# Performance work log

Measured on AMD Instinct MI355X. Metric: run time of the kernel, lower is better.

## Reference

```python
import jax, jax.numpy as jnp
import numpy as np

EPS = 1e-8

def setup_inputs() -> dict:
    key = jax.random.key(0)
    k0, k1, k2, k3, k4 = jax.random.split(key, 5)
    B, N, K, Q, L, F = 8, 5, 5, 4, 128, 768
    support_emb = jax.random.normal(k0, (B, N, K, L, F), dtype=jnp.float32)
    query_emb = jax.random.normal(k1, (B, N * Q, L, F), dtype=jnp.float32)
    B_mask = jax.random.randint(k2, (B, N, K, L), 0, 2, dtype=jnp.int32)
    I_mask = jax.random.randint(k3, (B, N, K, L), 0, 2, dtype=jnp.int32)
    trigger_label = jax.random.randint(k4, (B, N * Q, L), 0, 2 * N + 1, dtype=jnp.int32)
    return {"support_emb": support_emb, "query_emb": query_emb, "B_mask": B_mask,
            "I_mask": I_mask, "trigger_label": trigger_label, "N": N, "K": K, "Q": Q}

def _proto(support_emb, Bm, Im, N):
    # support_emb: (B,N,K,L,F); Bm/Im: (B,N,K,L) float
    sum_B = jnp.einsum('bnklf,bnkl->bnf', support_emb, Bm)
    cnt_B = Bm.sum((2, 3))[..., None] + EPS
    pB = sum_B / cnt_B                                   # (B,N,F)
    sum_I = jnp.einsum('bnklf,bnkl->bnf', support_emb, Im)
    cnt_I = Im.sum((2, 3))[..., None] + EPS
    pI = sum_I / cnt_I                                   # (B,N,F)
    Om = 1.0 - Bm - Im                                   # (B,N,K,L)
    sum_O = jnp.einsum('bnklf,bnkl->bf', support_emb, Om)
    cnt_O = Om.sum((1, 2, 3))[:, None] + EPS
    pO = sum_O / cnt_O                                   # (B,F)
    Bsz, F = pO.shape
    # interleave: tags [O, B_0, I_0, B_1, I_1, ...]
    pBI = jnp.stack([pB, pI], axis=2).reshape(Bsz, 2 * N, F)
    return jnp.concatenate([pO[:, None, :], pBI], axis=1)  # (B, 2N+1, F)

def reference(support_emb, query_emb, B_mask, I_mask, trigger_label, N, K, Q):
    dt = support_emb.dtype
    Bm = B_mask.astype(dt)
    Im = I_mask.astype(dt)
    prototype = _proto(support_emb, Bm, Im, N)             # (B, 2N+1, F)
    # similarity: broadcast dot product -> batched GEMM
    logits = jnp.einsum('bqlf,btf->bqlt', query_emb, prototype)  # (B, NQ, L, 2N+1)
    T = logits.shape[-1]
    flat = logits.reshape(-1, T)
    pred = jnp.argmax(flat, axis=1)
    lab = trigger_label.reshape(-1)
    logp = jax.nn.log_softmax(flat, axis=-1)
    loss = -jnp.take_along_axis(logp, lab[:, None], axis=1).mean()
    return (loss, logits, pred)
```

## Files before the change

### kernel.cpp

```cpp
#include <hip/hip_runtime.h>
#include <cstdint>
#include <cstddef>

#define EPS 1e-8f

#define Bsz 8
#define Nn  5
#define Kk  5
#define Ll  128
#define Ff  768
#define Tt  11
#define KL  640
#define ROWS_PER_B 2560
#define NROWS 20480
#define F4  192
#define BN  40

#define S1_ROWS 64
#define S1_CH   (KL / S1_ROWS)
#define S1_NBLK (BN * S1_CH)
#define PART_STRIDE (3 * Ff)
#define PART_STRIDE4 (PART_STRIDE / 4)

typedef float v2f __attribute__((ext_vector_type(2)));

__global__ __launch_bounds__(192) void stage1(
    const float* __restrict__ sup,
    const int*   __restrict__ Bm,
    const int*   __restrict__ Im,
    float* __restrict__ part,
    float* __restrict__ pcnt)
{
    int blk = blockIdx.x;
    int bn  = blk / S1_CH;
    int ch  = blk - bn * S1_CH;
    int tid = threadIdx.x;

    const float4* sp = (const float4*)(sup + ((size_t)bn * KL + ch * S1_ROWS) * Ff) + tid;
    const int*    bp = Bm + bn * KL + ch * S1_ROWS;
    const int*    ip = Im + bn * KL + ch * S1_ROWS;

    v2f tB0 = {0.f,0.f}, tB1 = tB0, tI0 = tB0, tI1 = tB0, tA0 = tB0, tA1 = tB0;
    int cB = 0, cI = 0;

    for (int h = 0; h < S1_ROWS / 8; ++h) {
        float4 v[8];
        #pragma unroll
        for (int j = 0; j < 8; ++j) v[j] = sp[(size_t)(h * 8 + j) * F4];
        #pragma unroll
        for (int j = 0; j < 8; ++j) {
            int p = h * 8 + j;
            v2f lo = {v[j].x, v[j].y};
            v2f hi = {v[j].z, v[j].w};
            tA0 += lo; tA1 += hi;
            if (bp[p]) { tB0 += lo; tB1 += hi; ++cB; }
            if (ip[p]) { tI0 += lo; tI1 += hi; ++cI; }
        }
    }

    float4* o = (float4*)(part + (size_t)blk * PART_STRIDE);
    float4 rB = {tB0.x, tB0.y, tB1.x, tB1.y};
    float4 rI = {tI0.x, tI0.y, tI1.x, tI1.y};
    float4 rA = {tA0.x, tA0.y, tA1.x, tA1.y};
    o[tid]          = rB;
    o[F4 + tid]     = rI;
    o[2 * F4 + tid] = rA;

    if (tid == 0) {
        pcnt[2 * (size_t)blk]     = (float)cB;
        pcnt[2 * (size_t)blk + 1] = (float)cI;
    }
}

__global__ __launch_bounds__(256) void stage2(
    const float* __restrict__ part,
    const float* __restrict__ pcnt,
    float* __restrict__ bnsum,
    float* __restrict__ cnt,
    float* __restrict__ loss_out)
{
    int gid = blockIdx.x * 256 + threadIdx.x;
    if (gid == 0) loss_out[0] = 0.0f;

    int bn  = gid / (3 * F4);
    int r   = gid - bn * (3 * F4);
    int set = r / F4;
    int f4  = r - set * F4;

    const float4* src = (const float4*)part + ((size_t)bn * S1_CH * 3 + set) * F4 + f4;
    float4 s = {0, 0, 0, 0};
    float4 v[S1_CH];
    #pragma unroll
    for (int c = 0; c < S1_CH; ++c) v[c] = src[(size_t)c * PART_STRIDE4];
    #pragma unroll
    for (int c = 0; c < S1_CH; ++c) {
        s.x += v[c].x; s.y += v[c].y; s.z += v[c].z; s.w += v[c].w;
    }
    ((float4*)bnsum)[((size_t)bn * 3 + set) * F4 + f4] = s;

    if (gid < 2 * BN) {
        int bn2  = gid >> 1;
        int set2 = gid & 1;
        float cv = 0.0f;
        #pragma unroll
        for (int c = 0; c < S1_CH; ++c) cv += pcnt[2 * ((size_t)bn2 * S1_CH + c) + set2];
        cnt[gid] = cv;
    }
}

__global__ __launch_bounds__(192) void stage2b(
    const float* __restrict__ bnsum,
    const float* __restrict__ cnt,
    float* __restrict__ proto)
{
    int b  = blockIdx.x / Tt;
    int t  = blockIdx.x - b * Tt;
    int f4 = threadIdx.x;

    const float4* bs = (const float4*)bnsum + (size_t)b * Nn * 3 * F4;

    float scale;
    if (t == 0) {
        float cO = (float)(KL * Nn);
        #pragma unroll
        for (int k = 0; k < 2 * Nn; ++k) cO -= cnt[2 * Nn * b + k];
        scale = 1.0f / (cO + EPS);
    } else {
        scale = 1.0f / (cnt[2 * Nn * b + (t - 1)] + EPS);
    }

    float4 val;
    if (t == 0) {
        float sx = 0, sy = 0, sz = 0, sw = 0;
        #pragma unroll
        for (int n = 0; n < Nn; ++n) {
            float4 A  = bs[(n * 3 + 2) * F4 + f4];
            float4 Bv = bs[(n * 3 + 0) * F4 + f4];
            float4 Iv = bs[(n * 3 + 1) * F4 + f4];
            sx += A.x - Bv.x - Iv.x; sy += A.y - Bv.y - Iv.y;
            sz += A.z - Bv.z - Iv.z; sw += A.w - Bv.w - Iv.w;
        }
        val.x = sx; val.y = sy; val.z = sz; val.w = sw;
    } else {
        int n  = (t - 1) >> 1;
        int st = (t - 1) & 1;
        val = bs[(n * 3 + st) * F4 + f4];
    }
    val.x *= scale; val.y *= scale; val.z *= scale; val.w *= scale;
    ((float4*)proto)[((size_t)b * Tt + t) * F4 + f4] = val;
}

#define S3_ROWS 64
#define S3_NBLK (NROWS / S3_ROWS)

__global__ __launch_bounds__(256) void stage3(
    const float* __restrict__ query,
    const float* __restrict__ proto,
    const int*   __restrict__ label,
    float* __restrict__ out_logits,
    float* __restrict__ out_pred,
    float* __restrict__ loss_out)
{
    __shared__ float4 ldsP[Tt * F4];
    __shared__ float  lred[4];

    int blk = blockIdx.x;
    int tid = threadIdx.x;
    int b   = blk / (ROWS_PER_B / S3_ROWS);

    const float4* pp = (const float4*)proto + (size_t)b * Tt * F4;
    for (int idx = tid; idx < Tt * F4; idx += 256) ldsP[idx] = pp[idx];
    __syncthreads();

    int p = tid >> 4;
    int s = tid & 15;

    size_t row0 = (size_t)blk * S3_ROWS + p * 4;
    const float4* qb = (const float4*)query + row0 * F4 + s;

    float a0[Tt], a1[Tt], a2[Tt], a3[Tt];
    #pragma unroll
    for (int t = 0; t < Tt; ++t) { a0[t] = 0.f; a1[t] = 0.f; a2[t] = 0.f; a3[t] = 0.f; }

    float4 u0 = qb[0 * F4], u1 = qb[1 * F4], u2 = qb[2 * F4], u3 = qb[3 * F4];

    const float4* pb = ldsP + s;
    #pragma unroll
    for (int j = 0; j < 12; ++j) {
        float4 w0, w1, w2, w3;
        if (j < 11) {
            int o = (j + 1) * 16;
            w0 = qb[0 * F4 + o]; w1 = qb[1 * F4 + o];
            w2 = qb[2 * F4 + o]; w3 = qb[3 * F4 + o];
        }
        #pragma unroll
        for (int t = 0; t < Tt; ++t) {
            float4 pv = pb[t * F4 + j * 16];
            float d0 = a0[t], d1 = a1[t], d2 = a2[t], d3 = a3[t];
            d0 = fmaf(u0.x, pv.x, d0); d0 = fmaf(u0.y, pv.y, d0);
            d0 = fmaf(u0.z, pv.z, d0); d0 = fmaf(u0.w, pv.w, d0);
            d1 = fmaf(u1.x, pv.x, d1); d1 = fmaf(u1.y, pv.y, d1);
            d1 = fmaf(u1.z, pv.z, d1); d1 = fmaf(u1.w, pv.w, d1);
            d2 = fmaf(u2.x, pv.x, d2); d2 = fmaf(u2.y, pv.y, d2);
            d2 = fmaf(u2.z, pv.z, d2); d2 = fmaf(u2.w, pv.w, d2);
            d3 = fmaf(u3.x, pv.x, d3); d3 = fmaf(u3.y, pv.y, d3);
            d3 = fmaf(u3.z, pv.z, d3); d3 = fmaf(u3.w, pv.w, d3);
            a0[t] = d0; a1[t] = d1; a2[t] = d2; a3[t] = d3;
        }
        if (j < 11) { u0 = w0; u1 = w1; u2 = w2; u3 = w3; }
    }

    #pragma unroll
    for (int t = 0; t < Tt; ++t) {
        a0[t] += __shfl_xor(a0[t], 1, 16); a0[t] += __shfl_xor(a0[t], 2, 16);
        a0[t] += __shfl_xor(a0[t], 4, 16); a0[t] += __shfl_xor(a0[t], 8, 16);
        a1[t] += __shfl_xor(a1[t], 1, 16); a1[t] += __shfl_xor(a1[t], 2, 16);
        a1[t] += __shfl_xor(a1[t], 4, 16); a1[t] += __shfl_xor(a1[t], 8, 16);
        a2[t] += __shfl_xor(a2[t], 1, 16); a2[t] += __shfl_xor(a2[t], 2, 16);
        a2[t] += __shfl_xor(a2[t], 4, 16); a2[t] += __shfl_xor(a2[t], 8, 16);
        a3[t] += __shfl_xor(a3[t], 1, 16); a3[t] += __shfl_xor(a3[t], 2, 16);
        a3[t] += __shfl_xor(a3[t], 4, 16); a3[t] += __shfl_xor(a3[t], 8, 16);
    }

    float wloss = 0.0f;
    if (s < 4) {
        float rv[Tt];
        #pragma unroll
        for (int t = 0; t < Tt; ++t)
            rv[t] = (s == 0) ? a0[t] : (s == 1) ? a1[t] : (s == 2) ? a2[t] : a3[t];
        size_t grow = row0 + s;

        float m = rv[0]; int bt = 0;
        #pragma unroll
        for (int t = 1; t < Tt; ++t) if (rv[t] > m) { m = rv[t]; bt = t; }
        float sum = 0.0f;
        #pragma unroll
        for (int t = 0; t < Tt; ++t) sum += __expf(rv[t] - m);
        int lab = label[grow];
        float labv = rv[0];
        #pragma unroll
        for (int t = 1; t < Tt; ++t) labv = (lab == t) ? rv[t] : labv;
        #pragma unroll
        for (int t = 0; t < Tt; ++t) out_logits[grow * Tt + t] = rv[t];
        out_pred[grow] = (float)bt;
        wloss = (m + __logf(sum)) - labv;
    }
    #pragma unroll
    for (int off = 32; off > 0; off >>= 1) wloss += __shfl_xor(wloss, off, 64);
    if ((tid & 63) == 0) lred[tid >> 6] = wloss;
    __syncthreads();
    if (tid == 0)
        atomicAdd(loss_out, (lred[0] + lred[1] + lred[2] + lred[3]) * (1.0f / (float)NROWS));
}

extern "C" void kernel_launch(void* const* d_in, const int* in_sizes, int n_in,
                              void* d_out, int out_size, void* d_ws, size_t ws_size,
                              hipStream_t stream) {
    const float* sup   = (const float*)d_in[0];
    const float* query = (const float*)d_in[1];
    const int*   Bm    = (const int*)d_in[2];
    const int*   Im    = (const int*)d_in[3];
    const int*   lab   = (const int*)d_in[4];

    float* w     = (float*)d_ws;
    float* part  = w;
    float* pcnt  = part + (size_t)S1_NBLK * PART_STRIDE;
    float* bnsum = pcnt + 2 * S1_NBLK;
    float* cnt   = bnsum + (size_t)BN * 3 * Ff;
    float* proto = cnt + 2 * BN;

    float* loss_out   = (float*)d_out;
    float* out_logits = (float*)d_out + 1;
    float* out_pred   = (float*)d_out + 1 + (size_t)NROWS * Tt;

    stage1<<<S1_NBLK, 192, 0, stream>>>(sup, Bm, Im, part, pcnt);
    stage2<<<90, 256, 0, stream>>>(part, pcnt, bnsum, cnt, loss_out);
    stage2b<<<Bsz * Tt, 192, 0, stream>>>(bnsum, cnt, proto);
    stage3<<<S3_NBLK, 256, 0, stream>>>(query, proto, lab,
                                        out_logits, out_pred, loss_out);
}
```

Baseline: 195.5 us.

## Widen stage1 blocks, fuse stage2 kernels, and raise stage3 rows per thread

Stage1 now runs four 192-thread row groups per block and reduces their partials in shared memory, giving more loads in flight per block. The two small prototype kernels are merged into one kernel that keeps per-batch sums in LDS, which removes a launch and a global round trip. Stage3 now has each thread accumulate 8 rows instead of 4 in 128-thread blocks, so each prototype value read from LDS is reused across twice as many rows. The cost is much higher register pressure in stage3 (88 accumulators plus 16 float4 query buffers), which could lower occupancy or cause spills.

Result: no change. 195.5 us, median of 2 (+0.0%).

```diff
diff --git a/kernel.cpp b/kernel.cpp
--- a/kernel.cpp
+++ b/kernel.cpp
@@ -17,6 +17,8 @@
 #define BN  40
 
 #define S1_ROWS 64
+#define S1_G    4
+#define S1_GR   16
 #define S1_CH   (KL / S1_ROWS)
 #define S1_NBLK (BN * S1_CH)
 #define PART_STRIDE (3 * Ff)
@@ -24,26 +26,33 @@
 
 typedef float v2f __attribute__((ext_vector_type(2)));
 
-__global__ __launch_bounds__(192) void stage1(
+__global__ __launch_bounds__(768) void stage1(
     const float* __restrict__ sup,
     const int*   __restrict__ Bm,
     const int*   __restrict__ Im,
     float* __restrict__ part,
     float* __restrict__ pcnt)
 {
+    __shared__ float4 red[S1_G * 3 * F4];
+    __shared__ float  redc[S1_G * 2];
+
     int blk = blockIdx.x;
     int bn  = blk / S1_CH;
     int ch  = blk - bn * S1_CH;
     int tid = threadIdx.x;
-
-    const float4* sp = (const float4*)(sup + ((size_t)bn * KL + ch * S1_ROWS) * Ff) + tid;
-    const int*    bp = Bm + bn * KL + ch * S1_ROWS;
-    const int*    ip = Im + bn * KL + ch * S1_ROWS;
+    int g   = tid / 192;
+    int col = tid - g * 192;
+    int rbase = ch * S1_ROWS + g * S1_GR;
+
+    const float4* sp = (const float4*)(sup + ((size_t)bn * KL + rbase) * Ff) + col;
+    const int*    bp = Bm + bn * KL + rbase;
+    const int*    ip = Im + bn * KL + rbase;
 
     v2f tB0 = {0.f,0.f}, tB1 = tB0, tI0 = tB0, tI1 = tB0, tA0 = tB0, tA1 = tB0;
     int cB = 0, cI = 0;
 
-    for (int h = 0; h < S1_ROWS / 8; ++h) {
+    #pragma unroll
+    for (int h = 0; h < S1_GR / 8; ++h) {
         float4 v[8];
         #pragma unroll
         for (int j = 0; j < 8; ++j) v[j] = sp[(size_t)(h * 8 + j) * F4];
@@ -58,102 +67,110 @@
         }
     }
 
-    float4* o = (float4*)(part + (size_t)blk * PART_STRIDE);
-    float4 rB = {tB0.x, tB0.y, tB1.x, tB1.y};
-    float4 rI = {tI0.x, tI0.y, tI1.x, tI1.y};
-    float4 rA = {tA0.x, tA0.y, tA1.x, tA1.y};
-    o[tid]          = rB;
-    o[F4 + tid]     = rI;
-    o[2 * F4 + tid] = rA;
-
+    red[(g * 3 + 0) * F4 + col] = (float4){tB0.x, tB0.y, tB1.x, tB1.y};
+    red[(g * 3 + 1) * F4 + col] = (float4){tI0.x, tI0.y, tI1.x, tI1.y};
+    red[(g * 3 + 2) * F4 + col] = (float4){tA0.x, tA0.y, tA1.x, tA1.y};
+    if (col == 0) { redc[g * 2] = (float)cB; redc[g * 2 + 1] = (float)cI; }
+    __syncthreads();
+
+    if (tid < 3 * F4) {
+        int set = tid / F4;
+        int c   = tid - set * F4;
+        float4 a = red[(0 * 3 + set) * F4 + c];
+        float4 b = red[(1 * 3 + set) * F4 + c];
+        float4 d = red[(2 * 3 + set) * F4 + c];
+        float4 e = red[(3 * 3 + set) * F4 + c];
+        float4 s = {a.x + b.x + d.x + e.x, a.y + b.y + d.y + e.y,
+                    a.z + b.z + d.z + e.z, a.w + b.w + d.w + e.w};
+        ((float4*)(part + (size_t)blk * PART_STRIDE))[tid] = s;
+    }
     if (tid == 0) {
-        pcnt[2 * (size_t)blk]     = (float)cB;
-        pcnt[2 * (size_t)blk + 1] = (float)cI;
+        pcnt[2 * (size_t)blk]     = redc[0] + redc[2] + redc[4] + redc[6];
+        pcnt[2 * (size_t)blk + 1] = redc[1] + redc[3] + redc[5] + redc[7];
     }
 }
 
-__global__ __launch_bounds__(256) void stage2(
+#define S2_Q  4
+#define S2_QF (F4 / S2_Q)
+
+__global__ __launch_bounds__(512) void stage2f(
     const float* __restrict__ part,
     const float* __restrict__ pcnt,
-    float* __restrict__ bnsum,
-    float* __restrict__ cnt,
+    float* __restrict__ proto,
     float* __restrict__ loss_out)
 {
-    int gid = blockIdx.x * 256 + threadIdx.x;
-    if (gid == 0) loss_out[0] = 0.0f;
-
-    int bn  = gid / (3 * F4);
-    int r   = gid - bn * (3 * F4);
-    int set = r / F4;
-    int f4  = r - set * F4;
-
-    const float4* src = (const float4*)part + ((size_t)bn * S1_CH * 3 + set) * F4 + f4;
-    float4 s = {0, 0, 0, 0};
-    float4 v[S1_CH];
-    #pragma unroll
-    for (int c = 0; c < S1_CH; ++c) v[c] = src[(size_t)c * PART_STRIDE4];
-    #pragma unroll
-    for (int c = 0; c < S1_CH; ++c) {
-        s.x += v[c].x; s.y += v[c].y; s.z += v[c].z; s.w += v[c].w;
-    }
-    ((float4*)bnsum)[((size_t)bn * 3 + set) * F4 + f4] = s;
-
-    if (gid < 2 * BN) {
-        int bn2  = gid >> 1;
-        int set2 = gid & 1;
+    __shared__ float4 bns[Nn * 3 * S2_QF];
+    __shared__ float  scnt[2 * Nn];
+
+    int blk = blockIdx.x;
+    int b   = blk / S2_Q;
+    int q   = blk - b * S2_Q;
+    int tid = threadIdx.x;
+
+    if (blk == 0 && tid == 0) loss_out[0] = 0.0f;
+
+    for (int it = tid; it < Nn * 3 * S2_QF; it += 512) {
+        int n   = it / (3 * S2_QF);
+        int r   = it - n * (3 * S2_QF);
+        int set = r / S2_QF;
+        int f   = r - set * S2_QF;
+        const float4* src = (const float4*)part
+            + ((size_t)((b * Nn + n) * S1_CH) * 3 + set) * F4 + (q * S2_QF + f);
+        float4 s = {0, 0, 0, 0};
+        float4 v[S1_CH];
+        #pragma unroll
+        for (int c = 0; c < S1_CH; ++c) v[c] = src[(size_t)c * PART_STRIDE4];
+        #pragma unroll
+        for (int c = 0; c < S1_CH; ++c) {
+            s.x += v[c].x; s.y += v[c].y; s.z += v[c].z; s.w += v[c].w;
+        }
+        bns[it] = s;
+    }
+    if (tid < 2 * Nn) {
+        int n = tid >> 1, set = tid & 1;
         float cv = 0.0f;
         #pragma unroll
-        for (int c = 0; c < S1_CH; ++c) cv += pcnt[2 * ((size_t)bn2 * S1_CH + c) + set2];
-        cnt[gid] = cv;
-    }
-}
-
-__global__ __launch_bounds__(192) void stage2b(
-    const float* __restrict__ bnsum,
-    const float* __restrict__ cnt,
-    float* __restrict__ proto)
-{
-    int b  = blockIdx.x / Tt;
-    int t  = blockIdx.x - b * Tt;
-    int f4 = threadIdx.x;
-
-    const float4* bs = (const float4*)bnsum + (size_t)b * Nn * 3 * F4;
-
-    float scale;
-    if (t == 0) {
-        float cO = (float)(KL * Nn);
-        #pragma unroll
-        for (int k = 0; k < 2 * Nn; ++k) cO -= cnt[2 * Nn * b + k];
-        scale = 1.0f / (cO + EPS);
-    } else {
-        scale = 1.0f / (cnt[2 * Nn * b + (t - 1)] + EPS);
-    }
-
-    float4 val;
-    if (t == 0) {
-        float sx = 0, sy = 0, sz = 0, sw = 0;
-        #pragma unroll
-        for (int n = 0; n < Nn; ++n) {
-            float4 A  = bs[(n * 3 + 2) * F4 + f4];
-            float4 Bv = bs[(n * 3 + 0) * F4 + f4];
-            float4 Iv = bs[(n * 3 + 1) * F4 + f4];
-            sx += A.x - Bv.x - Iv.x; sy += A.y - Bv.y - Iv.y;
-            sz += A.z - Bv.z - Iv.z; sw += A.w - Bv.w - Iv.w;
-        }
-        val.x = sx; val.y = sy; val.z = sz; val.w = sw;
-    } else {
-        int n  = (t - 1) >> 1;
-        int st = (t - 1) & 1;
-        val = bs[(n * 3 + st) * F4 + f4];
-    }
-    val.x *= scale; val.y *= scale; val.z *= scale; val.w *= scale;
-    ((float4*)proto)[((size_t)b * Tt + t) * F4 + f4] = val;
+        for (int c = 0; c < S1_CH; ++c)
+            cv += pcnt[2 * ((size_t)(b * Nn + n) * S1_CH + c) + set];
+        scnt[tid] = cv;
+    }
+    __syncthreads();
+
+    for (int it = tid; it < Tt * S2_QF; it += 512) {
+        int t = it / S2_QF;
+        int f = it - t * S2_QF;
+        float scale;
+        float4 val;
+        if (t == 0) {
+            float cO = (float)(KL * Nn);
+            #pragma unroll
+            for (int k = 0; k < 2 * Nn; ++k) cO -= scnt[k];
+            scale = 1.0f / (cO + EPS);
+            float sx = 0, sy = 0, sz = 0, sw = 0;
+            #pragma unroll
+            for (int n = 0; n < Nn; ++n) {
+                float4 A  = bns[(n * 3 + 2) * S2_QF + f];
+                float4 Bv = bns[(n * 3 + 0) * S2_QF + f];
+                float4 Iv = bns[(n * 3 + 1) * S2_QF + f];
+                sx += A.x - Bv.x - Iv.x; sy += A.y - Bv.y - Iv.y;
+                sz += A.z - Bv.z - Iv.z; sw += A.w - Bv.w - Iv.w;
+            }
+            val = (float4){sx, sy, sz, sw};
+        } else {
+            int n  = (t - 1) >> 1;
+            int st = (t - 1) & 1;
+            scale = 1.0f / (scnt[t - 1] + EPS);
+            val = bns[(n * 3 + st) * S2_QF + f];
+        }
+        val.x *= scale; val.y *= scale; val.z *= scale; val.w *= scale;
+        ((float4*)proto)[((size_t)b * Tt + t) * F4 + q * S2_QF + f] = val;
+    }
 }
 
 #define S3_ROWS 64
 #define S3_NBLK (NROWS / S3_ROWS)
 
-__global__ __launch_bounds__(256) void stage3(
+__global__ __launch_bounds__(128) void stage3(
     const float* __restrict__ query,
     const float* __restrict__ proto,
     const int*   __restrict__ label,
@@ -162,72 +179,82 @@
     float* __restrict__ loss_out)
 {
     __shared__ float4 ldsP[Tt * F4];
-    __shared__ float  lred[4];
+    __shared__ float  lred[2];
 
     int blk = blockIdx.x;
     int tid = threadIdx.x;
     int b   = blk / (ROWS_PER_B / S3_ROWS);
 
     const float4* pp = (const float4*)proto + (size_t)b * Tt * F4;
-    for (int idx = tid; idx < Tt * F4; idx += 256) ldsP[idx] = pp[idx];
+    for (int idx = tid; idx < Tt * F4; idx += 128) ldsP[idx] = pp[idx];
     __syncthreads();
 
     int p = tid >> 4;
     int s = tid & 15;
 
-    size_t row0 = (size_t)blk * S3_ROWS + p * 4;
+    size_t row0 = (size_t)blk * S3_ROWS + p * 8;
     const float4* qb = (const float4*)query + row0 * F4 + s;
 
-    float a0[Tt], a1[Tt], a2[Tt], a3[Tt];
-    #pragma unroll
-    for (int t = 0; t < Tt; ++t) { a0[t] = 0.f; a1[t] = 0.f; a2[t] = 0.f; a3[t] = 0.f; }
-
-    float4 u0 = qb[0 * F4], u1 = qb[1 * F4], u2 = qb[2 * F4], u3 = qb[3 * F4];
+    float a[8][Tt];
+    #pragma unroll
+    for (int r = 0; r < 8; ++r)
+        #pragma unroll
+        for (int t = 0; t < Tt; ++t) a[r][t] = 0.0f;
+
+    float4 u[8], w[8];
+    #pragma unroll
+    for (int r = 0; r < 8; ++r) u[r] = qb[r * F4];
 
     const float4* pb = ldsP + s;
-    #pragma unroll
-    for (int j = 0; j < 12; ++j) {
-        float4 w0, w1, w2, w3;
-        if (j < 11) {
-            int o = (j + 1) * 16;
-            w0 = qb[0 * F4 + o]; w1 = qb[1 * F4 + o];
-            w2 = qb[2 * F4 + o]; w3 = qb[3 * F4 + o];
-        }
+    for (int jj = 0; jj < 6; ++jj) {
+        int j0 = 2 * jj, j1 = 2 * jj + 1;
+        #pragma unroll
+        for (int r = 0; r < 8; ++r) w[r] = qb[r * F4 + j1 * 16];
         #pragma unroll
         for (int t = 0; t < Tt; ++t) {
-            float4 pv = pb[t * F4 + j * 16];
-            float d0 = a0[t], d1 = a1[t], d2 = a2[t], d3 = a3[t];
-            d0 = fmaf(u0.x, pv.x, d0); d0 = fmaf(u0.y, pv.y, d0);
-            d0 = fmaf(u0.z, pv.z, d0); d0 = fmaf(u0.w, pv.w, d0);
-            d1 = fmaf(u1.x, pv.x, d1); d1 = fmaf(u1.y, pv.y, d1);
-            d1 = fmaf(u1.z, pv.z, d1); d1 = fmaf(u1.w, pv.w, d1);
-            d2 = fmaf(u2.x, pv.x, d2); d2 = fmaf(u2.y, pv.y, d2);
-            d2 = fmaf(u2.z, pv.z, d2); d2 = fmaf(u2.w, pv.w, d2);
-            d3 = fmaf(u3.x, pv.x, d3); d3 = fmaf(u3.y, pv.y, d3);
-            d3 = fmaf(u3.z, pv.z, d3); d3 = fmaf(u3.w, pv.w, d3);
-            a0[t] = d0; a1[t] = d1; a2[t] = d2; a3[t] = d3;
-        }
-        if (j < 11) { u0 = w0; u1 = w1; u2 = w2; u3 = w3; }
-    }
-
-    #pragma unroll
-    for (int t = 0; t < Tt; ++t) {
-        a0[t] += __shfl_xor(a0[t], 1, 16); a0[t] += __shfl_xor(a0[t], 2, 16);
-        a0[t] += __shfl_xor(a0[t], 4, 16); a0[t] += __shfl_xor(a0[t], 8, 16);
-        a1[t] += __shfl_xor(a1[t], 1, 16); a1[t] += __shfl_xor(a1[t], 2, 16);
-        a1[t] += __shfl_xor(a1[t], 4, 16); a1[t] += __shfl_xor(a1[t], 8, 16);
-        a2[t] += __shfl_xor(a2[t], 1, 16); a2[t] += __shfl_xor(a2[t], 2, 16);
-        a2[t] += __shfl_xor(a2[t], 4, 16); a2[t] += __shfl_xor(a2[t], 8, 16);
-        a3[t] += __shfl_xor(a3[t], 1, 16); a3[t] += __shfl_xor(a3[t], 2, 16);
-        a3[t] += __shfl_xor(a3[t], 4, 16); a3[t] += __shfl_xor(a3[t], 8, 16);
-    }
+            float4 pv = pb[t * F4 + j0 * 16];
+            #pragma unroll
+            for (int r = 0; r < 8; ++r) {
+                float d = a[r][t];
+                d = fmaf(u[r].x, pv.x, d); d = fmaf(u[r].y, pv.y, d);
+                d = fmaf(u[r].z, pv.z, d); d = fmaf(u[r].w, pv.w, d);
+                a[r][t] = d;
+            }
+        }
+        int o2 = (jj < 5) ? (2 * jj + 2) * 16 : 0;
+        #pragma unroll
+        for (int r = 0; r < 8; ++r) u[r] = qb[r * F4 + o2];
+        #pragma unroll
+        for (int t = 0; t < Tt; ++t) {
+            float4 pv = pb[t * F4 + j1 * 16];
+            #pragma unroll
+            for (int r = 0; r < 8; ++r) {
+                float d = a[r][t];
+                d = fmaf(w[r].x, pv.x, d); d = fmaf(w[r].y, pv.y, d);
+                d = fmaf(w[r].z, pv.z, d); d = fmaf(w[r].w, pv.w, d);
+                a[r][t] = d;
+            }
+        }
+    }
+
+    #pragma unroll
+    for (int r = 0; r < 8; ++r)
+        #pragma unroll
+        for (int t = 0; t < Tt; ++t) {
+            float v = a[r][t];
+            v += __shfl_xor(v, 1, 16); v += __shfl_xor(v, 2, 16);
+            v += __shfl_xor(v, 4, 16); v += __shfl_xor(v, 8, 16);
+            a[r][t] = v;
+        }
 
     float wloss = 0.0f;
-    if (s < 4) {
+    if (s < 8) {
         float rv[Tt];
         #pragma unroll
         for (int t = 0; t < Tt; ++t)
-            rv[t] = (s == 0) ? a0[t] : (s == 1) ? a1[t] : (s == 2) ? a2[t] : a3[t];
+            rv[t] = (s == 0) ? a[0][t] : (s == 1) ? a[1][t] : (s == 2) ? a[2][t]
+                  : (s == 3) ? a[3][t] : (s == 4) ? a[4][t] : (s == 5) ? a[5][t]
+                  : (s == 6) ? a[6][t] : a[7][t];
         size_t grow = row0 + s;
 
         float m = rv[0]; int bt = 0;
@@ -250,7 +277,7 @@
     if ((tid & 63) == 0) lred[tid >> 6] = wloss;
     __syncthreads();
     if (tid == 0)
-        atomicAdd(loss_out, (lred[0] + lred[1] + lred[2] + lred[3]) * (1.0f / (float)NROWS));
+        atomicAdd(loss_out, (lred[0] + lred[1]) * (1.0f / (float)NROWS));
 }
 
 extern "C" void kernel_launch(void* const* d_in, const int* in_sizes, int n_in,
@@ -265,17 +292,14 @@
     float* w     = (float*)d_ws;
     float* part  = w;
     float* pcnt  = part + (size_t)S1_NBLK * PART_STRIDE;
-    float* bnsum = pcnt + 2 * S1_NBLK;
-    float* cnt   = bnsum + (size_t)BN * 3 * Ff;
-    float* proto = cnt + 2 * BN;
+    float* proto = pcnt + 2 * S1_NBLK;
 
     float* loss_out   = (float*)d_out;
     float* out_logits = (float*)d_out + 1;
     float* out_pred   = (float*)d_out + 1 + (size_t)NROWS * Tt;
 
-    stage1<<<S1_NBLK, 192, 0, stream>>>(sup, Bm, Im, part, pcnt);
-    stage2<<<90, 256, 0, stream>>>(part, pcnt, bnsum, cnt, loss_out);
-    stage2b<<<Bsz * Tt, 192, 0, stream>>>(bnsum, cnt, proto);
-    stage3<<<S3_NBLK, 256, 0, stream>>>(query, proto, lab,
+    stage1<<<S1_NBLK, 768, 0, stream>>>(sup, Bm, Im, part, pcnt);
+    stage2f<<<Bsz * S2_Q, 512, 0, stream>>>(part, pcnt, proto, loss_out);
+    stage3<<<S3_NBLK, 128, 0, stream>>>(query, proto, lab,
                                         out_logits, out_pred, loss_out);
 }
```
